# Optimization experiments

Measured on AMD Instinct MI355X. Metric: run time of the kernel, lower is better.

## Reference

```python
import jax, jax.numpy as jnp
import numpy as np

NUM_HEADS = 16
NUM_BUCKETS = 32
MAX_DISTANCE = 128


def _rel_bucket(rel):
    # bidirectional T5-style relative position bucketing
    nb = NUM_BUCKETS // 2
    ret = (rel > 0).astype(jnp.int32) * nb
    n = jnp.abs(rel)
    max_exact = nb // 2
    is_small = n < max_exact
    safe = jnp.maximum(n, 1).astype(jnp.float32)
    large = max_exact + (jnp.log(safe / max_exact) / np.log(MAX_DISTANCE / max_exact) * (nb - max_exact)).astype(jnp.int32)
    large = jnp.minimum(large, nb - 1)
    return ret + jnp.where(is_small, n, large)


def setup_inputs() -> dict:
    key = jax.random.key(0)
    ks = jax.random.split(key, 12)
    S, B, E = 1024, 4, 1024
    D = E // NUM_HEADS
    s = 0.02
    return {
        "query": jax.random.normal(ks[0], (S, B, E), jnp.float32),
        "q_w": jax.random.normal(ks[1], (E, E), jnp.float32) * s,
        "q_b": jnp.zeros((E,), jnp.float32),
        "k_w": jax.random.normal(ks[2], (E, E), jnp.float32) * s,
        "k_b": jnp.zeros((E,), jnp.float32),
        "v_w": jax.random.normal(ks[3], (E, E), jnp.float32) * s,
        "v_b": jnp.zeros((E,), jnp.float32),
        "out_w": jax.random.normal(ks[4], (E, E), jnp.float32) * s,
        "out_b": jnp.zeros((E,), jnp.float32),
        "rel_emb": jax.random.normal(ks[5], (NUM_BUCKETS, NUM_HEADS), jnp.float32) * s,
        "grep_w": jax.random.normal(ks[6], (8, D), jnp.float32) * s,
        "grep_b": jnp.zeros((8,), jnp.float32),
        "grep_a": jnp.ones((NUM_HEADS,), jnp.float32),
    }


def reference(query, q_w, q_b, k_w, k_b, v_w, v_b, out_w, out_b, rel_emb, grep_w, grep_b, grep_a):
    S, B, E = query.shape
    H = NUM_HEADS
    D = E // H
    scaling = D ** -0.5

    q = (query @ q_w.T + q_b) * scaling  # scaling applied before gating, as in WavLM
    k = query @ k_w.T + k_b
    v = query @ v_w.T + v_b

    def split(x):  # (S,B,E) -> (B,H,S,D)
        return x.reshape(S, B, H, D).transpose(1, 2, 0, 3)

    q4, k4, v4 = split(q), split(k), split(v)

    attn = jnp.einsum('bhqd,bhkd->bhqk', q4, k4)  # (B,H,S,S)

    pos = jnp.arange(S)
    bucket = _rel_bucket(pos[None, :] - pos[:, None])  # (S,S)
    pbias = rel_emb[bucket].transpose(2, 0, 1)          # (H,S,S)

    # GRU-gated relative position scaling
    g = jnp.einsum('bhsd,ed->bhse', q4, grep_w) + grep_b      # (B,H,S,8)
    g = jax.nn.sigmoid(g.reshape(B, H, S, 2, 4).sum(-1))     # (B,H,S,2)
    gate_a, gate_b = g[..., 0], g[..., 1]
    gate = gate_a * (gate_b * grep_a[None, :, None] - 1.0) + 2.0  # (B,H,S)

    attn = attn + gate[..., None] * pbias[None]
    probs = jax.nn.softmax(attn, axis=-1)
    ctx = jnp.einsum('bhqk,bhkd->bhqd', probs, v4)  # (B,H,S,D)
    out = ctx.transpose(2, 0, 1, 3).reshape(S, B, E) @ out_w.T + out_b
    return out
```

## Files before the change

kernel.cpp:

```cpp
#include <hip/hip_runtime.h>
#include <hip/hip_bf16.h>
#include <stdint.h>


typedef short bf16x8 __attribute__((ext_vector_type(8)));
typedef _Float16 f16x8 __attribute__((ext_vector_type(8)));
typedef float f32x4 __attribute__((ext_vector_type(4)));
typedef float f32x16 __attribute__((ext_vector_type(16)));

#define MFMA_BF16(a, b, c) __builtin_amdgcn_mfma_f32_16x16x32_bf16((a), (b), (c), 0, 0, 0)
#define MFMA_F16(a, b, c) __builtin_amdgcn_mfma_f32_16x16x32_f16((a), (b), (c), 0, 0, 0)
#define MFMA32_BF16(a, b, c) __builtin_amdgcn_mfma_f32_32x32x16_bf16((a), (b), (c), 0, 0, 0)

#define LOG2E 1.44269504088896f
#define LN2 0.693147180559945f

__device__ __forceinline__ unsigned short f2bf(float x) {
  union { float f; unsigned u; } v; v.f = x;
  unsigned r = v.u + 0x7fffu + ((v.u >> 16) & 1u);
  return (unsigned short)(r >> 16);
}
__device__ __forceinline__ float bf2f(unsigned short u) {
  union { unsigned u; float f; } v; v.u = ((unsigned)u) << 16;
  return v.f;
}
__device__ __forceinline__ unsigned short f2h(float x) {
  union { _Float16 h; unsigned short u; } v; v.h = (_Float16)x;
  return v.u;
}
__device__ __forceinline__ float u32lo_bf(unsigned u) {
  union { unsigned u; float f; } v; v.u = u << 16;
  return v.f;
}
__device__ __forceinline__ float u32hi_bf(unsigned u) {
  union { unsigned u; float f; } v; v.u = u & 0xffff0000u;
  return v.f;
}
__device__ __forceinline__ unsigned pk_bf2(float a, float b) {
  union { __hip_bfloat162 h2; unsigned u; } v;
  v.h2 = __float22bfloat162_rn(float2{a, b});
  return v.u;
}

__device__ __forceinline__ void gload_lds16(const void* g, void* l) {
  __builtin_amdgcn_global_load_lds(
      (const __attribute__((address_space(1))) unsigned int*)g,
      (__attribute__((address_space(3))) unsigned int*)l, 16, 0, 0);
}

__device__ __forceinline__ int swz(int row) { return (row ^ (row >> 2)) & 3; }

__global__ __launch_bounds__(256) void prep_kernel(
    const float* __restrict__ query, const float* __restrict__ q_w,
    const float* __restrict__ k_w, const float* __restrict__ v_w,
    const float* __restrict__ out_w, const float* __restrict__ rel_emb,
    unsigned short* __restrict__ q_bf, unsigned short* __restrict__ wq,
    unsigned short* __restrict__ wk, unsigned short* __restrict__ wv,
    unsigned short* __restrict__ ow_h,
    unsigned short* __restrict__ bias_hd) {
  int i = blockIdx.x * 256 + threadIdx.x;
  if (i < 4194304) {
    int e = i & 1023;
    int sb = i >> 10;
    int s = sb >> 2, b = sb & 3;
    q_bf[((size_t)(b * 1024 + s) << 10) | e] = f2bf(query[i]);
  } else if (i < 5242880) {
    int j = i - 4194304;
    wq[j] = f2bf(q_w[j]);
    wk[j] = f2bf(k_w[j]);
    wv[j] = f2bf(v_w[j]);
    ow_h[j] = f2h(out_w[j]);
  } else {
    int idx = i - 5242880;
    if (idx >= 2056) return;
    if (idx >= 2047) {
#pragma unroll
      for (int h = 0; h < 16; ++h) bias_hd[h * 2056 + idx] = 0;
      return;
    }
    int rel = idx - 1023;
    int n = rel < 0 ? -rel : rel;
    int ret = rel > 0 ? 16 : 0;
    int bucket;
    if (n < 8) {
      bucket = ret + n;
    } else {
      int large = 8 + (int)(logf((float)n / 8.0f) / logf(16.0f) * 8.0f);
      if (large > 15) large = 15;
      bucket = ret + large;
    }
#pragma unroll
    for (int h = 0; h < 16; ++h)
      bias_hd[h * 2056 + idx] = f2bf(rel_emb[bucket * 16 + h] * LOG2E);
  }
}

__global__ __launch_bounds__(256, 3) void qkv_gemm_kernel(
    const unsigned short* __restrict__ A, const unsigned short* __restrict__ Wq,
    const unsigned short* __restrict__ Wk, const unsigned short* __restrict__ Wv,
    const float* __restrict__ qb, const float* __restrict__ kb, const float* __restrict__ vb,
    unsigned short* __restrict__ qh,
    unsigned short* __restrict__ kh,
    unsigned short* __restrict__ vT)
{
  __shared__ __align__(16) char smem[32768];
  const int tid = threadIdx.x, lane = tid & 63;
  const int wv_ = tid >> 6;
  const int nt = blockIdx.x;
  const int mt = blockIdx.y;
  const int mat = nt >> 3;
  const unsigned short* W = mat == 0 ? Wq : (mat == 1 ? Wk : Wv);
  const int n0 = (nt & 7) * 128;
  const int m0 = mt * 128;
  const int moff = (wv_ & 1) * 64;
  const int noff = (wv_ >> 1) * 64;

  f32x4 acc[4][4] = {};
  const char* Ab = (const char*)A;
  const char* Wb = (const char*)W;

  int st_row[2], st_g[2];
#pragma unroll
  for (int c = 0; c < 2; ++c) {
    int o = c * 4096 + tid * 16;
    int row = o >> 6, p = (o >> 4) & 3;
    st_row[c] = row;
    st_g[c] = p ^ swz(row);
  }

#define QKV_STAGE(kt, buf)                                                     \
  {                                                                            \
    char* bb = smem + (buf)*16384;                                             \
    _Pragma("unroll") for (int c = 0; c < 2; ++c) {                            \
      int o = c * 4096 + tid * 16;                                             \
      size_t ga = (size_t)(m0 + st_row[c]) * 2048 + (size_t)(kt)*64 + st_g[c] * 16; \
      size_t gb = (size_t)(n0 + st_row[c]) * 2048 + (size_t)(kt)*64 + st_g[c] * 16; \
      gload_lds16(Ab + ga, bb + o);                                            \
      gload_lds16(Wb + gb, bb + 8192 + o);                                     \
    }                                                                          \
  }

  QKV_STAGE(0, 0);
  for (int kt = 0; kt < 32; ++kt) {
    __syncthreads();
    const char* base = smem + (kt & 1) * 16384;
    if (kt < 31) QKV_STAGE(kt + 1, (kt + 1) & 1);

    bf16x8 af[4], bfr[4];
#pragma unroll
    for (int i = 0; i < 4; ++i) {
      int ra = moff + i * 16 + (lane & 15);
      int rb = noff + i * 16 + (lane & 15);
      int q = lane >> 4;
      af[i] = *(const bf16x8*)(base + ra * 64 + (q ^ swz(ra)) * 16);
      bfr[i] = *(const bf16x8*)(base + 8192 + rb * 64 + (q ^ swz(rb)) * 16);
    }
#pragma unroll
    for (int i = 0; i < 4; ++i)
#pragma unroll
      for (int j = 0; j < 4; ++j) acc[i][j] = MFMA_BF16(af[i], bfr[j], acc[i][j]);
  }
#undef QKV_STAGE

  const int bidx = m0 >> 10;
  const int s00 = (m0 & 1023) + moff + ((lane >> 4) << 2);
  const int c0 = n0 + noff + (lane & 15);
  if (mat < 2) {
    const float* barr = mat == 0 ? qb : kb;
    unsigned short* dst = mat == 0 ? qh : kh;
    const float scale = mat == 0 ? (0.125f * LOG2E) : 1.0f;
#pragma unroll
    for (int j = 0; j < 4; ++j) {
      int col = c0 + j * 16;
      int hh = col >> 6, dd = col & 63;
      float bias = barr[col];
#pragma unroll
      for (int i = 0; i < 4; ++i)
#pragma unroll
        for (int r = 0; r < 4; ++r) {
          int s = s00 + i * 16 + r;
          dst[((size_t)(bidx * 16 + hh) * 1024 + s) * 64 + dd] =
              f2bf((acc[i][j][r] + bias) * scale);
        }
    }
  } else {
#pragma unroll
    for (int j = 0; j < 4; ++j) {
      int col = c0 + j * 16;
      int hh = col >> 6, dd = col & 63;
      float bias = vb[col];
#pragma unroll
      for (int i = 0; i < 4; ++i) {
        int s = s00 + i * 16;
        ushort4 pk;
        pk.x = f2bf(acc[i][j][0] + bias);
        pk.y = f2bf(acc[i][j][1] + bias);
        pk.z = f2bf(acc[i][j][2] + bias);
        pk.w = f2bf(acc[i][j][3] + bias);
        *(ushort4*)&vT[((size_t)(bidx * 16 + hh) * 64 + dd) * 1024 + s] = pk;
      }
    }
  }
}

__global__ __launch_bounds__(256) void gate_kernel(const unsigned short* __restrict__ qh,
                                                   const float* __restrict__ grep_w,
                                                   const float* __restrict__ grep_b,
                                                   const float* __restrict__ grep_a,
                                                   float* __restrict__ gate) {
  __shared__ float gw[512];
  __shared__ float gbb[8];
  __shared__ float gaa[16];
  int tid = threadIdx.x;
  for (int i = tid; i < 512; i += 256) gw[i] = grep_w[i];
  if (tid < 8) gbb[tid] = grep_b[tid];
  if (tid < 16) gaa[tid] = grep_a[tid];
  __syncthreads();
  int idx = blockIdx.x * 256 + tid;
  int h = (idx >> 10) & 15;
  const unsigned short* qrow = qh + (size_t)idx * 64;
  float a[8] = {0.f, 0.f, 0.f, 0.f, 0.f, 0.f, 0.f, 0.f};
#pragma unroll
  for (int c = 0; c < 8; ++c) {
    bf16x8 v = *(const bf16x8*)(qrow + c * 8);
#pragma unroll
    for (int jj = 0; jj < 8; ++jj) {
      float qv = bf2f((unsigned short)v[jj]);
      int d = c * 8 + jj;
#pragma unroll
      for (int e = 0; e < 8; ++e) a[e] += qv * gw[e * 64 + d];
    }
  }
  float sa = (a[0] + a[1] + a[2] + a[3]) * LN2 + gbb[0] + gbb[1] + gbb[2] + gbb[3];
  float sb = (a[4] + a[5] + a[6] + a[7]) * LN2 + gbb[4] + gbb[5] + gbb[6] + gbb[7];
  float siga = 1.f / (1.f + __expf(-sa));
  float sigb = 1.f / (1.f + __expf(-sb));
  gate[idx] = siga * (sigb * gaa[h] - 1.f) + 2.f;
}

__global__ __launch_bounds__(512, 4) void attn_kernel(
    const unsigned short* __restrict__ qh, const unsigned short* __restrict__ kh,
    const unsigned short* __restrict__ vT, const float* __restrict__ gate,
    const unsigned short* __restrict__ bias_hd, unsigned short* __restrict__ ctx) {
  __shared__ __align__(16) char smem[37888];
  const int tid = threadIdx.x, lane = tid & 63, w = tid >> 6;
  const int qt = w >> 1, khalf = w & 1;
  const int bh = blockIdx.x;
  const int h = bh & 15;
  const int qs0 = blockIdx.y * 128;
  const int q31 = lane & 31, hb = lane >> 5, q7 = q31 & 7;
  const int sq = qs0 + qt * 32 + q31;

  unsigned short* bc0 = (unsigned short*)(smem + 33280);
  unsigned short* bc1 = (unsigned short*)(smem + 35584);
  {
    const unsigned short* gb = bias_hd + h * 2056 + (896 - qs0);
    for (int i = tid; i < 1152; i += 512) {
      bc0[i] = gb[i];
      bc1[i] = gb[i + 1];
    }
  }

  const char* kbase = (const char*)(kh + (size_t)bh * 65536);
  const char* vbase = (const char*)(vT + (size_t)bh * 65536);

  const int o = tid * 16;
  const int srow = o >> 7;
  const int sg = ((o >> 4) & 7) ^ (srow & 7);
  const size_t koff = (size_t)srow * 128 + sg * 16;
  const size_t voff = (size_t)srow * 2048 + sg * 16;

  gload_lds16(kbase + koff, smem + o);
  gload_lds16(vbase + voff, smem + 16384 + o);

  const unsigned short* qrow = qh + ((size_t)bh * 1024 + sq) * 64 + hb * 8;
  bf16x8 qf[4];
#pragma unroll
  for (int dc = 0; dc < 4; ++dc) qf[dc] = *(const bf16x8*)(qrow + dc * 16);

  const float gate_lane = gate[bh * 1024 + sq];

  const int par = (127 - q31) & 1;
  const unsigned int* bp = (const unsigned int*)(par ? bc1 : bc0);
  const int bbase0 = (qs0 + 127 - sq - par) >> 1;

  float l_run = 0.f;
  f32x16 accO0 = {}, accO1 = {};

  for (int kc = 0; kc < 16; ++kc) {
    __syncthreads();
    const char* Kc = smem + (kc & 1) * 8192;
    const char* Vc = smem + 16384 + (kc & 1) * 8192;
    if (kc < 15) {
      int nb = (kc + 1) & 1;
      gload_lds16(kbase + (size_t)(kc + 1) * 8192 + koff, smem + nb * 8192 + o);
      gload_lds16(vbase + (size_t)(kc + 1) * 128 + voff, smem + 16384 + nb * 8192 + o);
    }

    f32x16 sac = {};
    const char* Krow = Kc + (khalf * 32 + q31) * 128;
#pragma unroll
    for (int ks = 0; ks < 4; ++ks) {
      bf16x8 kf = *(const bf16x8*)(Krow + (((ks * 2 + hb) ^ q7) << 4));
      sac = MFMA32_BF16(kf, qf[ks], sac);
    }

    float ps = 0.f;
    unsigned pu[8];
#pragma unroll
    for (int rg = 0; rg < 4; ++rg) {
      int idx = bbase0 + ((kc * 64 + khalf * 32 + rg * 8 + hb * 4) >> 1);
      unsigned u0 = bp[idx], u1 = bp[idx + 1];
      float p0 = __builtin_exp2f(__builtin_fmaf(gate_lane, u32lo_bf(u0), sac[rg * 4 + 0]));
      float p1 = __builtin_exp2f(__builtin_fmaf(gate_lane, u32hi_bf(u0), sac[rg * 4 + 1]));
      float p2 = __builtin_exp2f(__builtin_fmaf(gate_lane, u32lo_bf(u1), sac[rg * 4 + 2]));
      float p3 = __builtin_exp2f(__builtin_fmaf(gate_lane, u32hi_bf(u1), sac[rg * 4 + 3]));
      ps += (p0 + p1) + (p2 + p3);
      pu[2 * rg] = pk_bf2(p0, p1);
      pu[2 * rg + 1] = pk_bf2(p2, p3);
    }
    l_run += ps;

    unsigned s0a = hb ? pu[0] : pu[2], s0b = hb ? pu[1] : pu[3];
    unsigned s1a = hb ? pu[4] : pu[6], s1b = hb ? pu[5] : pu[7];
    unsigned r0a = __shfl_xor((int)s0a, 32, 64);
    unsigned r0b = __shfl_xor((int)s0b, 32, 64);
    unsigned r1a = __shfl_xor((int)s1a, 32, 64);
    unsigned r1b = __shfl_xor((int)s1b, 32, 64);
    union PB { unsigned u[4]; bf16x8 v; } b0, b1;
    b0.u[0] = hb ? r0a : pu[0];
    b0.u[1] = hb ? r0b : pu[1];
    b0.u[2] = hb ? pu[2] : r0a;
    b0.u[3] = hb ? pu[3] : r0b;
    b1.u[0] = hb ? r1a : pu[4];
    b1.u[1] = hb ? r1b : pu[5];
    b1.u[2] = hb ? pu[6] : r1a;
    b1.u[3] = hb ? pu[7] : r1b;

#pragma unroll
    for (int mf = 0; mf < 2; ++mf) {
      bf16x8 pb = mf ? b1.v : b0.v;
      int vch = ((khalf * 4 + mf * 2 + hb) ^ q7) << 4;
      bf16x8 v0f = *(const bf16x8*)(Vc + q31 * 128 + vch);
      bf16x8 v1f = *(const bf16x8*)(Vc + (32 + q31) * 128 + vch);
      accO0 = MFMA32_BF16(v0f, pb, accO0);
      accO1 = MFMA32_BF16(v1f, pb, accO1);
    }
  }

  l_run += __shfl_xor(l_run, 32, 64);

  __syncthreads();
  float* Ot = (float*)smem;
  float* ow = Ot + (qt * 32 + q31) * 65;
  if (khalf == 0) {
#pragma unroll
    for (int rr = 0; rr < 16; ++rr) {
      int d = (rr & 3) + 8 * (rr >> 2) + 4 * hb;
      ow[d] = accO0[rr];
      ow[32 + d] = accO1[rr];
    }
    if (hb == 0) ow[64] = l_run;
  }
  __syncthreads();
  if (khalf == 1) {
    float inv = 1.0f / (ow[64] + l_run);
#pragma unroll
    for (int rr = 0; rr < 16; ++rr) {
      int d = (rr & 3) + 8 * (rr >> 2) + 4 * hb;
      ow[d] = (ow[d] + accO0[rr]) * inv;
      ow[32 + d] = (ow[32 + d] + accO1[rr]) * inv;
    }
  }
  __syncthreads();
  {
    int row = tid >> 2, dg = tid & 3;
    int s = qs0 + row;
    const float* src = Ot + row * 65 + dg * 16;
    unsigned short hbuf[16];
#pragma unroll
    for (int j = 0; j < 16; ++j) hbuf[j] = f2h(src[j]);
    size_t base = (size_t)(s * 4 + (bh >> 4)) * 1024 + h * 64 + dg * 16;
    *(uint4*)(ctx + base) = *(const uint4*)(hbuf);
    *(uint4*)(ctx + base + 8) = *(const uint4*)(hbuf + 8);
  }
}

__global__ __launch_bounds__(256, 3) void outproj_kernel(
    const unsigned short* __restrict__ Af,
    const unsigned short* __restrict__ Bf,
    const float* __restrict__ ob, float* __restrict__ out) {
  __shared__ __align__(16) char smem[24576];
  const int tid = threadIdx.x, lane = tid & 63, wv_ = tid >> 6;
  const int q15 = lane & 15, quad = lane >> 4;
  const int n0 = blockIdx.x * 128;
  const int m0 = blockIdx.y * 64;
  const int moff = (wv_ & 1) * 32;
  const int noff = (wv_ >> 1) * 64;

  const int oa = tid * 16;
  const int ra_ = oa >> 6;
  const int ga_ = (((oa >> 4) & 3) ^ swz(ra_)) << 4;
  int rb_[2], gb_[2], obo_[2];
#pragma unroll
  for (int c = 0; c < 2; ++c) {
    int ob2 = c * 4096 + tid * 16;
    obo_[c] = ob2;
    rb_[c] = ob2 >> 6;
    gb_[c] = (((ob2 >> 4) & 3) ^ swz(rb_[c])) << 4;
  }

#define OP_STAGE(kt, buf)                                                        \
  {                                                                              \
    char* bb = smem + (buf)*12288;                                               \
    size_t ga = (size_t)(m0 + ra_) * 2048 + (size_t)(kt)*64 + ga_;               \
    gload_lds16((const char*)Af + ga, bb + oa);                                  \
    _Pragma("unroll") for (int c = 0; c < 2; ++c) {                              \
      size_t gb = (size_t)(n0 + rb_[c]) * 2048 + (size_t)(kt)*64 + gb_[c];       \
      gload_lds16((const char*)Bf + gb, bb + 4096 + obo_[c]);                    \
    }                                                                            \
  }

  f32x4 acc[2][4] = {};
  OP_STAGE(0, 0);
  for (int kt = 0; kt < 32; ++kt) {
    __syncthreads();
    const char* base = smem + (kt & 1) * 12288;
    if (kt < 31) OP_STAGE(kt + 1, (kt + 1) & 1);

    f16x8 ah[2], bhf[4];
#pragma unroll
    for (int i = 0; i < 2; ++i) {
      int ra = moff + i * 16 + q15;
      ah[i] = *(const f16x8*)(base + ra * 64 + ((quad ^ swz(ra)) << 4));
    }
#pragma unroll
    for (int j = 0; j < 4; ++j) {
      int rb = noff + j * 16 + q15;
      bhf[j] = *(const f16x8*)(base + 4096 + rb * 64 + ((quad ^ swz(rb)) << 4));
    }
#pragma unroll
    for (int i = 0; i < 2; ++i)
#pragma unroll
      for (int j = 0; j < 4; ++j) acc[i][j] = MFMA_F16(ah[i], bhf[j], acc[i][j]);
  }
#undef OP_STAGE

  const int rr0 = m0 + moff + (quad << 2);
  const int c0 = n0 + noff + q15;
#pragma unroll
  for (int j = 0; j < 4; ++j) {
    int col = c0 + j * 16;
    float bias = ob[col];
#pragma unroll
    for (int i = 0; i < 2; ++i)
#pragma unroll
      for (int r = 0; r < 4; ++r)
        out[(size_t)(rr0 + i * 16 + r) * 1024 + col] = acc[i][j][r] + bias;
  }
}

extern "C" void kernel_launch(void* const* d_in, const int* in_sizes, int n_in,
                              void* d_out, int out_size, void* d_ws, size_t ws_size,
                              hipStream_t stream) {
  const float* query = (const float*)d_in[0];
  const float* q_w = (const float*)d_in[1];
  const float* q_b = (const float*)d_in[2];
  const float* k_w = (const float*)d_in[3];
  const float* k_b = (const float*)d_in[4];
  const float* v_w = (const float*)d_in[5];
  const float* v_b = (const float*)d_in[6];
  const float* out_w = (const float*)d_in[7];
  const float* out_b = (const float*)d_in[8];
  const float* rel_emb = (const float*)d_in[9];
  const float* grep_w = (const float*)d_in[10];
  const float* grep_b = (const float*)d_in[11];
  const float* grep_a = (const float*)d_in[12];
  float* out = (float*)d_out;

  const size_t MB = 1u << 20;
  char* ws = (char*)d_ws;
  unsigned short* q_bf = (unsigned short*)(ws);
  unsigned short* wq_bf = (unsigned short*)(ws + 8 * MB);
  unsigned short* wk_bf = (unsigned short*)(ws + 10 * MB);
  unsigned short* wv_bf = (unsigned short*)(ws + 12 * MB);
  unsigned short* ow_h = (unsigned short*)(ws + 14 * MB);
  unsigned short* qhp = (unsigned short*)(ws + 16 * MB);
  unsigned short* khp = (unsigned short*)(ws + 24 * MB);
  unsigned short* vTp = (unsigned short*)(ws + 32 * MB);
  unsigned short* ctxp = (unsigned short*)(ws + 40 * MB);
  float* gatep = (float*)(ws + 48 * MB);
  unsigned short* biasp = (unsigned short*)(ws + 48 * MB + 256 * 1024);

  prep_kernel<<<20489, 256, 0, stream>>>(query, q_w, k_w, v_w, out_w, rel_emb, q_bf, wq_bf,
                                         wk_bf, wv_bf, ow_h, biasp);
  qkv_gemm_kernel<<<dim3(24, 32), 256, 0, stream>>>(q_bf, wq_bf, wk_bf, wv_bf, q_b, k_b, v_b,
                                                    qhp, khp, vTp);
  gate_kernel<<<256, 256, 0, stream>>>(qhp, grep_w, grep_b, grep_a, gatep);
  attn_kernel<<<dim3(64, 8), 512, 0, stream>>>(qhp, khp, vTp, gatep, biasp, ctxp);
  outproj_kernel<<<dim3(8, 64), 256, 0, stream>>>(ctxp, ow_h, out_b, out);
}
```

Baseline: 194.5 us.

## Vectorize prep casts, transpose GEMM epilogues, use fp32 bias and permlane swaps

The prep kernel now converts four elements per thread with float4 loads and ushort4 stores. The QKV and output-projection GEMMs swap operand roles so each lane holds contiguous columns, which allows packed 8- or 16-byte epilogue stores. The attention kernel keeps the relative-position bias in fp32 in LDS, folds the gated bias into the accumulator initialisation, and replaces the shuffle/select exchange with permlane32_swap. The changes target memory-instruction count and ALU overhead, at the cost of extra LDS reads for the bias and a different accumulator layout.

```diff
diff --git a/kernel.cpp b/kernel.cpp
--- a/kernel.cpp
+++ b/kernel.cpp
@@ -7,6 +7,7 @@
 typedef _Float16 f16x8 __attribute__((ext_vector_type(8)));
 typedef float f32x4 __attribute__((ext_vector_type(4)));
 typedef float f32x16 __attribute__((ext_vector_type(16)));
+typedef unsigned uint32x2 __attribute__((ext_vector_type(2)));
 
 #define MFMA_BF16(a, b, c) __builtin_amdgcn_mfma_f32_16x16x32_bf16((a), (b), (c), 0, 0, 0)
 #define MFMA_F16(a, b, c) __builtin_amdgcn_mfma_f32_16x16x32_f16((a), (b), (c), 0, 0, 0)
@@ -27,14 +28,6 @@
 __device__ __forceinline__ unsigned short f2h(float x) {
   union { _Float16 h; unsigned short u; } v; v.h = (_Float16)x;
   return v.u;
-}
-__device__ __forceinline__ float u32lo_bf(unsigned u) {
-  union { unsigned u; float f; } v; v.u = u << 16;
-  return v.f;
-}
-__device__ __forceinline__ float u32hi_bf(unsigned u) {
-  union { unsigned u; float f; } v; v.u = u & 0xffff0000u;
-  return v.f;
 }
 __device__ __forceinline__ unsigned pk_bf2(float a, float b) {
   union { __hip_bfloat162 h2; unsigned u; } v;
@@ -57,25 +50,37 @@
     unsigned short* __restrict__ q_bf, unsigned short* __restrict__ wq,
     unsigned short* __restrict__ wk, unsigned short* __restrict__ wv,
     unsigned short* __restrict__ ow_h,
-    unsigned short* __restrict__ bias_hd) {
+    float* __restrict__ bias_f) {
   int i = blockIdx.x * 256 + threadIdx.x;
-  if (i < 4194304) {
-    int e = i & 1023;
-    int sb = i >> 10;
+  if (i < 1048576) {
+    int e4 = (i & 255) << 2;
+    int sb = i >> 8;
     int s = sb >> 2, b = sb & 3;
-    q_bf[((size_t)(b * 1024 + s) << 10) | e] = f2bf(query[i]);
-  } else if (i < 5242880) {
-    int j = i - 4194304;
-    wq[j] = f2bf(q_w[j]);
-    wk[j] = f2bf(k_w[j]);
-    wv[j] = f2bf(v_w[j]);
-    ow_h[j] = f2h(out_w[j]);
+    float4 q4 = *(const float4*)(query + ((size_t)i << 2));
+    ushort4 o;
+    o.x = f2bf(q4.x); o.y = f2bf(q4.y); o.z = f2bf(q4.z); o.w = f2bf(q4.w);
+    *(ushort4*)&q_bf[((size_t)(b * 1024 + s) << 10) | e4] = o;
+  } else if (i < 1310720) {
+    int j = (i - 1048576) << 2;
+    float4 a = *(const float4*)(q_w + j);
+    float4 b = *(const float4*)(k_w + j);
+    float4 c = *(const float4*)(v_w + j);
+    float4 d = *(const float4*)(out_w + j);
+    ushort4 o;
+    o.x = f2bf(a.x); o.y = f2bf(a.y); o.z = f2bf(a.z); o.w = f2bf(a.w);
+    *(ushort4*)&wq[j] = o;
+    o.x = f2bf(b.x); o.y = f2bf(b.y); o.z = f2bf(b.z); o.w = f2bf(b.w);
+    *(ushort4*)&wk[j] = o;
+    o.x = f2bf(c.x); o.y = f2bf(c.y); o.z = f2bf(c.z); o.w = f2bf(c.w);
+    *(ushort4*)&wv[j] = o;
+    o.x = f2h(d.x); o.y = f2h(d.y); o.z = f2h(d.z); o.w = f2h(d.w);
+    *(ushort4*)&ow_h[j] = o;
   } else {
-    int idx = i - 5242880;
+    int idx = i - 1310720;
     if (idx >= 2056) return;
     if (idx >= 2047) {
 #pragma unroll
-      for (int h = 0; h < 16; ++h) bias_hd[h * 2056 + idx] = 0;
+      for (int h = 0; h < 16; ++h) bias_f[h * 2056 + idx] = 0.f;
       return;
     }
     int rel = idx - 1023;
@@ -91,7 +96,7 @@
     }
 #pragma unroll
     for (int h = 0; h < 16; ++h)
-      bias_hd[h * 2056 + idx] = f2bf(rel_emb[bucket * 16 + h] * LOG2E);
+      bias_f[h * 2056 + idx] = rel_emb[bucket * 16 + h] * LOG2E;
   }
 }
 
@@ -114,6 +119,12 @@
   const int m0 = mt * 128;
   const int moff = (wv_ & 1) * 64;
   const int noff = (wv_ >> 1) * 64;
+  const int q15 = lane & 15, quad = lane >> 4;
+
+  const int abase = (mat < 2) ? 8192 : 0;
+  const int bbase2 = 8192 - abase;
+  const int aoff = (mat < 2) ? noff : moff;
+  const int boff = (mat < 2) ? moff : noff;
 
   f32x4 acc[4][4] = {};
   const char* Ab = (const char*)A;
@@ -149,11 +160,10 @@
     bf16x8 af[4], bfr[4];
 #pragma unroll
     for (int i = 0; i < 4; ++i) {
-      int ra = moff + i * 16 + (lane & 15);
-      int rb = noff + i * 16 + (lane & 15);
-      int q = lane >> 4;
-      af[i] = *(const bf16x8*)(base + ra * 64 + (q ^ swz(ra)) * 16);
-      bfr[i] = *(const bf16x8*)(base + 8192 + rb * 64 + (q ^ swz(rb)) * 16);
+      int ra = aoff + i * 16 + q15;
+      int rb = boff + i * 16 + q15;
+      af[i] = *(const bf16x8*)(base + abase + ra * 64 + ((quad ^ swz(ra)) << 4));
+      bfr[i] = *(const bf16x8*)(base + bbase2 + rb * 64 + ((quad ^ swz(rb)) << 4));
     }
 #pragma unroll
     for (int i = 0; i < 4; ++i)
@@ -163,27 +173,34 @@
 #undef QKV_STAGE
 
   const int bidx = m0 >> 10;
-  const int s00 = (m0 & 1023) + moff + ((lane >> 4) << 2);
-  const int c0 = n0 + noff + (lane & 15);
   if (mat < 2) {
     const float* barr = mat == 0 ? qb : kb;
     unsigned short* dst = mat == 0 ? qh : kh;
     const float scale = mat == 0 ? (0.125f * LOG2E) : 1.0f;
-#pragma unroll
-    for (int j = 0; j < 4; ++j) {
-      int col = c0 + j * 16;
-      int hh = col >> 6, dd = col & 63;
-      float bias = barr[col];
-#pragma unroll
-      for (int i = 0; i < 4; ++i)
-#pragma unroll
-        for (int r = 0; r < 4; ++r) {
-          int s = s00 + i * 16 + r;
-          dst[((size_t)(bidx * 16 + hh) * 1024 + s) * 64 + dd] =
-              f2bf((acc[i][j][r] + bias) * scale);
-        }
+    const int sA = (m0 & 1023) + moff + q15;
+    const int nA = n0 + noff + (quad << 2);
+#pragma unroll
+    for (int i = 0; i < 4; ++i) {
+      int colb = nA + i * 16;
+      int hh = colb >> 6, dd = colb & 63;
+      float bs0 = barr[colb + 0] * scale;
+      float bs1 = barr[colb + 1] * scale;
+      float bs2 = barr[colb + 2] * scale;
+      float bs3 = barr[colb + 3] * scale;
+#pragma unroll
+      for (int j = 0; j < 4; ++j) {
+        int s = sA + j * 16;
+        ushort4 pk;
+        pk.x = f2bf(__builtin_fmaf(acc[i][j][0], scale, bs0));
+        pk.y = f2bf(__builtin_fmaf(acc[i][j][1], scale, bs1));
+        pk.z = f2bf(__builtin_fmaf(acc[i][j][2], scale, bs2));
+        pk.w = f2bf(__builtin_fmaf(acc[i][j][3], scale, bs3));
+        *(ushort4*)&dst[((size_t)(bidx * 16 + hh) * 1024 + s) * 64 + dd] = pk;
+      }
     }
   } else {
+    const int s00 = (m0 & 1023) + moff + (quad << 2);
+    const int c0 = n0 + noff + q15;
 #pragma unroll
     for (int j = 0; j < 4; ++j) {
       int col = c0 + j * 16;
@@ -241,7 +258,7 @@
 __global__ __launch_bounds__(512, 4) void attn_kernel(
     const unsigned short* __restrict__ qh, const unsigned short* __restrict__ kh,
     const unsigned short* __restrict__ vT, const float* __restrict__ gate,
-    const unsigned short* __restrict__ bias_hd, unsigned short* __restrict__ ctx) {
+    const float* __restrict__ bias_f, unsigned short* __restrict__ ctx) {
   __shared__ __align__(16) char smem[37888];
   const int tid = threadIdx.x, lane = tid & 63, w = tid >> 6;
   const int qt = w >> 1, khalf = w & 1;
@@ -251,14 +268,10 @@
   const int q31 = lane & 31, hb = lane >> 5, q7 = q31 & 7;
   const int sq = qs0 + qt * 32 + q31;
 
-  unsigned short* bc0 = (unsigned short*)(smem + 33280);
-  unsigned short* bc1 = (unsigned short*)(smem + 35584);
+  float* bcf = (float*)(smem + 33280);
   {
-    const unsigned short* gb = bias_hd + h * 2056 + (896 - qs0);
-    for (int i = tid; i < 1152; i += 512) {
-      bc0[i] = gb[i];
-      bc1[i] = gb[i + 1];
-    }
+    const float* gb = bias_f + h * 2056 + (896 - qs0);
+    for (int i = tid; i < 1152; i += 512) bcf[i] = gb[i];
   }
 
   const char* kbase = (const char*)(kh + (size_t)bh * 65536);
@@ -280,9 +293,7 @@
 
   const float gate_lane = gate[bh * 1024 + sq];
 
-  const int par = (127 - q31) & 1;
-  const unsigned int* bp = (const unsigned int*)(par ? bc1 : bc0);
-  const int bbase0 = (qs0 + 127 - sq - par) >> 1;
+  const int i0 = (qs0 + 127 - sq) + khalf * 32 + hb * 4;
 
   float l_run = 0.f;
   f32x16 accO0 = {}, accO1 = {};
@@ -297,7 +308,18 @@
       gload_lds16(vbase + (size_t)(kc + 1) * 128 + voff, smem + 16384 + nb * 8192 + o);
     }
 
-    f32x16 sac = {};
+    f32x16 sac;
+    {
+      const int ib = i0 + kc * 64;
+#pragma unroll
+      for (int rg = 0; rg < 4; ++rg) {
+        sac[rg * 4 + 0] = gate_lane * bcf[ib + rg * 8 + 0];
+        sac[rg * 4 + 1] = gate_lane * bcf[ib + rg * 8 + 1];
+        sac[rg * 4 + 2] = gate_lane * bcf[ib + rg * 8 + 2];
+        sac[rg * 4 + 3] = gate_lane * bcf[ib + rg * 8 + 3];
+      }
+    }
+
     const char* Krow = Kc + (khalf * 32 + q31) * 128;
 #pragma unroll
     for (int ks = 0; ks < 4; ++ks) {
@@ -309,33 +331,23 @@
     unsigned pu[8];
 #pragma unroll
     for (int rg = 0; rg < 4; ++rg) {
-      int idx = bbase0 + ((kc * 64 + khalf * 32 + rg * 8 + hb * 4) >> 1);
-      unsigned u0 = bp[idx], u1 = bp[idx + 1];
-      float p0 = __builtin_exp2f(__builtin_fmaf(gate_lane, u32lo_bf(u0), sac[rg * 4 + 0]));
-      float p1 = __builtin_exp2f(__builtin_fmaf(gate_lane, u32hi_bf(u0), sac[rg * 4 + 1]));
-      float p2 = __builtin_exp2f(__builtin_fmaf(gate_lane, u32lo_bf(u1), sac[rg * 4 + 2]));
-      float p3 = __builtin_exp2f(__builtin_fmaf(gate_lane, u32hi_bf(u1), sac[rg * 4 + 3]));
+      float p0 = __builtin_exp2f(sac[rg * 4 + 0]);
+      float p1 = __builtin_exp2f(sac[rg * 4 + 1]);
+      float p2 = __builtin_exp2f(sac[rg * 4 + 2]);
+      float p3 = __builtin_exp2f(sac[rg * 4 + 3]);
       ps += (p0 + p1) + (p2 + p3);
       pu[2 * rg] = pk_bf2(p0, p1);
       pu[2 * rg + 1] = pk_bf2(p2, p3);
     }
     l_run += ps;
 
-    unsigned s0a = hb ? pu[0] : pu[2], s0b = hb ? pu[1] : pu[3];
-    unsigned s1a = hb ? pu[4] : pu[6], s1b = hb ? pu[5] : pu[7];
-    unsigned r0a = __shfl_xor((int)s0a, 32, 64);
-    unsigned r0b = __shfl_xor((int)s0b, 32, 64);
-    unsigned r1a = __shfl_xor((int)s1a, 32, 64);
-    unsigned r1b = __shfl_xor((int)s1b, 32, 64);
+    uint32x2 s02 = __builtin_amdgcn_permlane32_swap(pu[0], pu[2], false, false);
+    uint32x2 s13 = __builtin_amdgcn_permlane32_swap(pu[1], pu[3], false, false);
+    uint32x2 s46 = __builtin_amdgcn_permlane32_swap(pu[4], pu[6], false, false);
+    uint32x2 s57 = __builtin_amdgcn_permlane32_swap(pu[5], pu[7], false, false);
     union PB { unsigned u[4]; bf16x8 v; } b0, b1;
-    b0.u[0] = hb ? r0a : pu[0];
-    b0.u[1] = hb ? r0b : pu[1];
-    b0.u[2] = hb ? pu[2] : r0a;
-    b0.u[3] = hb ? pu[3] : r0b;
-    b1.u[0] = hb ? r1a : pu[4];
-    b1.u[1] = hb ? r1b : pu[5];
-    b1.u[2] = hb ? pu[6] : r1a;
-    b1.u[3] = hb ? pu[7] : r1b;
+    b0.u[0] = s02.x; b0.u[1] = s13.x; b0.u[2] = s02.y; b0.u[3] = s13.y;
+    b1.u[0] = s46.x; b1.u[1] = s57.x; b1.u[2] = s46.y; b1.u[3] = s57.y;
 
 #pragma unroll
     for (int mf = 0; mf < 2; ++mf) {
@@ -421,42 +433,47 @@
     }                                                                            \
   }
 
-  f32x4 acc[2][4] = {};
+  f32x4 acc[4][2] = {};
   OP_STAGE(0, 0);
   for (int kt = 0; kt < 32; ++kt) {
     __syncthreads();
     const char* base = smem + (kt & 1) * 12288;
     if (kt < 31) OP_STAGE(kt + 1, (kt + 1) & 1);
 
-    f16x8 ah[2], bhf[4];
-#pragma unroll
-    for (int i = 0; i < 2; ++i) {
-      int ra = moff + i * 16 + q15;
-      ah[i] = *(const f16x8*)(base + ra * 64 + ((quad ^ swz(ra)) << 4));
-    }
-#pragma unroll
-    for (int j = 0; j < 4; ++j) {
-      int rb = noff + j * 16 + q15;
-      bhf[j] = *(const f16x8*)(base + 4096 + rb * 64 + ((quad ^ swz(rb)) << 4));
-    }
-#pragma unroll
-    for (int i = 0; i < 2; ++i)
-#pragma unroll
-      for (int j = 0; j < 4; ++j) acc[i][j] = MFMA_F16(ah[i], bhf[j], acc[i][j]);
+    f16x8 wf[4], cf[2];
+#pragma unroll
+    for (int i = 0; i < 4; ++i) {
+      int rb = noff + i * 16 + q15;
+      wf[i] = *(const f16x8*)(base + 4096 + rb * 64 + ((quad ^ swz(rb)) << 4));
+    }
+#pragma unroll
+    for (int j = 0; j < 2; ++j) {
+      int ra = moff + j * 16 + q15;
+      cf[j] = *(const f16x8*)(base + ra * 64 + ((quad ^ swz(ra)) << 4));
+    }
+#pragma unroll
+    for (int i = 0; i < 4; ++i)
+#pragma unroll
+      for (int j = 0; j < 2; ++j) acc[i][j] = MFMA_F16(wf[i], cf[j], acc[i][j]);
   }
 #undef OP_STAGE
 
-  const int rr0 = m0 + moff + (quad << 2);
-  const int c0 = n0 + noff + q15;
-#pragma unroll
-  for (int j = 0; j < 4; ++j) {
-    int col = c0 + j * 16;
-    float bias = ob[col];
-#pragma unroll
-    for (int i = 0; i < 2; ++i)
-#pragma unroll
-      for (int r = 0; r < 4; ++r)
-        out[(size_t)(rr0 + i * 16 + r) * 1024 + col] = acc[i][j][r] + bias;
+  const int sA = m0 + moff + q15;
+  const int nA = n0 + noff + (quad << 2);
+#pragma unroll
+  for (int i = 0; i < 4; ++i) {
+    int colb = nA + i * 16;
+    float4 b4 = *(const float4*)&ob[colb];
+#pragma unroll
+    for (int j = 0; j < 2; ++j) {
+      int s = sA + j * 16;
+      float4 o4;
+      o4.x = acc[i][j][0] + b4.x;
+      o4.y = acc[i][j][1] + b4.y;
+      o4.z = acc[i][j][2] + b4.z;
+      o4.w = acc[i][j][3] + b4.w;
+      *(float4*)&out[(size_t)s * 1024 + colb] = o4;
+    }
   }
 }
 
@@ -490,10 +507,10 @@
   unsigned short* vTp = (unsigned short*)(ws + 32 * MB);
   unsigned short* ctxp = (unsigned short*)(ws + 40 * MB);
   float* gatep = (float*)(ws + 48 * MB);
-  unsigned short* biasp = (unsigned short*)(ws + 48 * MB + 256 * 1024);
-
-  prep_kernel<<<20489, 256, 0, stream>>>(query, q_w, k_w, v_w, out_w, rel_emb, q_bf, wq_bf,
-                                         wk_bf, wv_bf, ow_h, biasp);
+  float* biasp = (float*)(ws + 48 * MB + 256 * 1024);
+
+  prep_kernel<<<5129, 256, 0, stream>>>(query, q_w, k_w, v_w, out_w, rel_emb, q_bf, wq_bf,
+                                        wk_bf, wv_bf, ow_h, biasp);
   qkv_gemm_kernel<<<dim3(24, 32), 256, 0, stream>>>(q_bf, wq_bf, wk_bf, wv_bf, q_b, k_b, v_b,
                                                     qhp, khp, vTp);
   gate_kernel<<<256, 256, 0, stream>>>(qhp, grep_w, grep_b, grep_a, gatep);
```

After: 193.0 us. Within noise of the previous version (-0.8%).
